# Kernel optimization log

Measured on AMD Instinct MI355X. Metric: run time of the kernel, lower is better.

Reference implementation:

```python
import jax, jax.numpy as jnp
import numpy as np

NUM_QUBITS = 10
LAYERS = 8
DIM = 2 ** NUM_QUBITS  # 1024


def _build_entangling(nq: int) -> jnp.ndarray:
    """Static chain-of-CNOTs entangling block, D x D complex64."""
    I = np.eye(2)
    cnot = np.array([[1, 0, 0, 0], [0, 1, 0, 0], [0, 0, 0, 1], [0, 0, 1, 0]], dtype=np.float64)
    M = np.eye(2 ** nq)
    layers = []
    for i in range(nq - 1):
        mats = [I] * nq
        mats[i] = cnot
        del mats[i + 1]
        out = np.eye(1)
        for m in mats:
            out = np.kron(out, m)
        layers.append(out)
    for L in reversed(layers):
        M = L @ M
    return jnp.asarray(M, dtype=jnp.complex64)


ENTANGLING = _build_entangling(NUM_QUBITS)


def _r3(angles):
    # angles: [B, 3] (omega, theta, phi) -> [B, 2, 2] complex64 R3 gate
    omega, theta, phi = angles[:, 0], angles[:, 1], angles[:, 2]
    c = jnp.cos(theta / 2).astype(jnp.complex64)
    s = jnp.sin(theta / 2).astype(jnp.complex64)
    m11 = jnp.exp(-0.5j * (phi + omega)) * c
    m12 = -jnp.exp(0.5j * (phi - omega)) * s
    m21 = jnp.exp(-0.5j * (phi - omega)) * s
    m22 = jnp.exp(0.5j * (phi + omega)) * c
    return jnp.stack([jnp.stack([m11, m12], -1), jnp.stack([m21, m22], -1)], -2)


def _batched_kron(a, b):
    # a: [B, m, n], b: [B, p, q] -> [B, m*p, n*q]
    B = a.shape[0]
    return jnp.einsum('bij,bkl->bikjl', a, b).reshape(B, a.shape[1] * b.shape[1], a.shape[2] * b.shape[2])


def _rotation_block(angles):
    # angles: [copies, num_qubits, 3] -> [copies, D, D] complex64
    out = _r3(angles[:, 0])
    for q in range(1, NUM_QUBITS):
        out = _batched_kron(out, _r3(angles[:, q]))
    return out


def setup_inputs() -> dict:
    key = jax.random.key(0)
    k1, k2 = jax.random.split(key)
    inp = jax.random.normal(k1, (128, DIM), dtype=jnp.float32)
    params = jax.random.normal(k2, (32, LAYERS, NUM_QUBITS, 3), dtype=jnp.float32)
    return {"input": inp, "params": params}


def reference(input, params):
    copies = params.shape[0]
    batch = input.shape[0] // copies
    M0 = jnp.broadcast_to(jnp.eye(DIM, dtype=jnp.complex64), (copies, DIM, DIM))
    xs = jnp.moveaxis(params, 1, 0)  # [layers, copies, nq, 3]

    def step(M, p):
        M = jnp.matmul(_rotation_block(p), M)         # rotation layer
        M = jnp.einsum('ij,bjk->bik', ENTANGLING, M)  # entangling layer
        return M, None

    M, _ = jax.lax.scan(step, M0, xs)
    M = jnp.repeat(M, batch, axis=0)                  # [copies*batch, D, D]
    x = input.astype(jnp.complex64)
    return jnp.einsum('bij,bj->bi', M, x)
```

## Files before the change

kernel.cpp:

```cpp
#include <hip/hip_runtime.h>


#define DIM 1024
#define NQ 10
#define NLAYERS 8
#define NGATES 80

__device__ __forceinline__ unsigned short f2bf(float f) {
    unsigned int u = __float_as_uint(f);
    unsigned int r = u + 0x7FFFu + ((u >> 16) & 1u);
    return (unsigned short)(r >> 16);
}

__device__ __forceinline__ float2 cmadd2(float2 c0, float2 x0, float2 c1, float2 x1) {
    float re = c0.x * x0.x - c0.y * x0.y + c1.x * x1.x - c1.y * x1.y;
    float im = c0.x * x0.y + c0.y * x0.x + c1.x * x1.y + c1.y * x1.x;
    return make_float2(re, im);
}

template <int K>
__device__ __forceinline__ void local_gate(float2 (&a)[4], float2 m11, float2 m12,
                                           float2 m21, float2 m22) {
#pragma unroll
    for (int p = 0; p < 2; ++p) {
        const int i0 = ((p >> K) << (K + 1)) | (p & ((1 << K) - 1));
        const int i1 = i0 | (1 << K);
        const float2 a0 = a[i0], a1 = a[i1];
        a[i0] = cmadd2(m11, a0, m12, a1);
        a[i1] = cmadd2(m21, a0, m22, a1);
    }
}

template <int M>
__device__ __forceinline__ void cross_gate(float2 (&a)[4], int lane, float2 m11,
                                           float2 m12, float2 m21, float2 m22) {
    const bool hi = (lane >> M) & 1;
    const float2 cs = hi ? m22 : m11;
    const float2 co = hi ? m21 : m12;
#pragma unroll
    for (int r = 0; r < 4; ++r) {
        float2 o;
        o.x = __shfl_xor(a[r].x, 1 << M, 64);
        o.y = __shfl_xor(a[r].y, 1 << M, 64);
        a[r] = cmadd2(cs, a[r], co, o);
    }
}

__global__ __launch_bounds__(256) void
UnitaryR3Ansatz_18846316495450_kernel(const float* __restrict__ inp,
                                      const float* __restrict__ params,
                                      void* __restrict__ outp,
                                      int out_size)
{
    __shared__ float4 gates[NGATES][2];
    __shared__ float4 stA[DIM / 2];
    __shared__ float4 stB[DIM / 2];

    const int b = blockIdx.x;
    const int c = b >> 2;
    const int tid = threadIdx.x;
    const int lane = tid & 63;

    if (tid < NGATES) {
        const float* p = params + c * (NGATES * 3) + tid * 3;
        const float omega = p[0], theta = p[1], phi = p[2];
        float sh, ch;  sincosf(0.5f * theta, &sh, &ch);
        float sa, ca;  sincosf(0.5f * (phi + omega), &sa, &ca);
        float sb, cb;  sincosf(0.5f * (phi - omega), &sb, &cb);
        gates[tid][0] = make_float4(ca * ch, -sa * ch, -cb * sh, -sb * sh);
        gates[tid][1] = make_float4(cb * sh, -sb * sh, ca * ch, sa * ch);
    }

    float2 a[4];
    {
        const float4 v = ((const float4*)(inp + b * DIM))[tid];
        a[0] = make_float2(v.x, 0.f);
        a[1] = make_float2(v.y, 0.f);
        a[2] = make_float2(v.z, 0.f);
        a[3] = make_float2(v.w, 0.f);
    }

    const int xb = tid << 2;
    int zb = xb;
    zb ^= zb >> 1; zb ^= zb >> 2; zb ^= zb >> 4; zb ^= zb >> 8;
    const int  zmid = zb & 0xFC;
    const bool z8 = (zb >> 8) & 1;
    const bool z9 = (zb >> 9) & 1;
    const bool s0 = zb & 1;
    const bool s1 = zb & 2;

    __syncthreads();

    float4* buf = stA;
    for (int l = 0; l < NLAYERS; ++l) {
        float2 m11, m12, m21, m22;
#define LOADG(q) { const float4 g0 = gates[l * NQ + (q)][0]; \
                   const float4 g1 = gates[l * NQ + (q)][1]; \
                   m11 = make_float2(g0.x, g0.y); m12 = make_float2(g0.z, g0.w); \
                   m21 = make_float2(g1.x, g1.y); m22 = make_float2(g1.z, g1.w); }
        LOADG(9); local_gate<0>(a, m11, m12, m21, m22);
        LOADG(8); local_gate<1>(a, m11, m12, m21, m22);
        LOADG(7); cross_gate<0>(a, lane, m11, m12, m21, m22);
        LOADG(6); cross_gate<1>(a, lane, m11, m12, m21, m22);
        LOADG(5); cross_gate<2>(a, lane, m11, m12, m21, m22);
        LOADG(4); cross_gate<3>(a, lane, m11, m12, m21, m22);
        LOADG(3); cross_gate<4>(a, lane, m11, m12, m21, m22);
        LOADG(2); cross_gate<5>(a, lane, m11, m12, m21, m22);

        buf[tid * 2]     = make_float4(a[0].x, a[0].y, a[1].x, a[1].y);
        buf[tid * 2 + 1] = make_float4(a[2].x, a[2].y, a[3].x, a[3].y);
        __syncthreads();

        LOADG(1);
        const float2 h0 = z8 ? m21 : m11;
        const float2 h1 = z8 ? m22 : m12;
        LOADG(0);
        const float2 g0r = z9 ? m21 : m11;
        const float2 g1r = z9 ? m22 : m12;
#undef LOADG

        float2 v0[4], v1[4];
        {
            const float4 p0 = buf[(zmid) >> 1],          p1 = buf[((zmid) >> 1) + 1];
            const float4 q0 = buf[(0x100 | zmid) >> 1],  q1 = buf[((0x100 | zmid) >> 1) + 1];
            v0[0] = cmadd2(h0, make_float2(p0.x, p0.y), h1, make_float2(q0.x, q0.y));
            v0[1] = cmadd2(h0, make_float2(p0.z, p0.w), h1, make_float2(q0.z, q0.w));
            v0[2] = cmadd2(h0, make_float2(p1.x, p1.y), h1, make_float2(q1.x, q1.y));
            v0[3] = cmadd2(h0, make_float2(p1.z, p1.w), h1, make_float2(q1.z, q1.w));
        }
        {
            const float4 p0 = buf[(0x200 | zmid) >> 1],  p1 = buf[((0x200 | zmid) >> 1) + 1];
            const float4 q0 = buf[(0x300 | zmid) >> 1],  q1 = buf[((0x300 | zmid) >> 1) + 1];
            v1[0] = cmadd2(h0, make_float2(p0.x, p0.y), h1, make_float2(q0.x, q0.y));
            v1[1] = cmadd2(h0, make_float2(p0.z, p0.w), h1, make_float2(q0.z, q0.w));
            v1[2] = cmadd2(h0, make_float2(p1.x, p1.y), h1, make_float2(q1.x, q1.y));
            v1[3] = cmadd2(h0, make_float2(p1.z, p1.w), h1, make_float2(q1.z, q1.w));
        }
        float2 u[4];
#pragma unroll
        for (int j = 0; j < 4; ++j) u[j] = cmadd2(g0r, v0[j], g1r, v1[j]);

        const float2 w0 = s0 ? u[1] : u[0];
        const float2 w1 = s0 ? u[0] : u[1];
        const float2 w2 = s0 ? u[3] : u[2];
        const float2 w3 = s0 ? u[2] : u[3];
        a[0] = s1 ? w2 : w0;
        a[1] = s1 ? w3 : w1;
        a[2] = s1 ? w1 : w3;
        a[3] = s1 ? w0 : w2;

        buf = (l & 1) ? stA : stB;
    }

    if (out_size >= 2 * DIM * 128) {
        ushort2* o2 = (ushort2*)outp + (size_t)b * DIM + tid * 4;
#pragma unroll
        for (int i = 0; i < 4; ++i) {
            ushort2 v; v.x = f2bf(a[i].x); v.y = f2bf(a[i].y);
            o2[i] = v;
        }
    } else {
        ((float4*)((float*)outp + (size_t)b * DIM))[tid] =
            make_float4(a[0].x, a[1].x, a[2].x, a[3].x);
    }
}

extern "C" void kernel_launch(void* const* d_in, const int* in_sizes, int n_in,
                              void* d_out, int out_size, void* d_ws, size_t ws_size,
                              hipStream_t stream) {
    const float* inp    = (const float*)d_in[0];
    const float* params = (const float*)d_in[1];
    (void)in_sizes; (void)n_in; (void)d_ws; (void)ws_size;
    UnitaryR3Ansatz_18846316495450_kernel<<<128, 256, 0, stream>>>(inp, params, d_out, out_size);
}
```

Baseline: 69.86 us.

## Use DPP/swizzle lane exchanges, halve gate storage, swizzle LDS staging

Replaces the generic shuffle-XOR lane exchanges with DPP quad/row operations and ds_swizzle for the small strides, which avoids the LDS-routed bpermute path. Stores only the first row of each R3 gate and derives the second row from the unitary's symmetry, halving shared gate loads. Applies an XOR swizzle to the staging buffer indices to reduce LDS bank conflicts on the float4 accesses. The kernel is tiny and launch-bound (128 blocks), so total gains may be small, and the DPP row_ror/swizzle encodings must match the intended xor patterns exactly.

```diff
diff --git a/kernel.cpp b/kernel.cpp
--- a/kernel.cpp
+++ b/kernel.cpp
@@ -5,6 +5,8 @@
 #define NQ 10
 #define NLAYERS 8
 #define NGATES 80
+
+#define SWZ(j) ((j) ^ (((j) >> 3) & 1))
 
 __device__ __forceinline__ unsigned short f2bf(float f) {
     unsigned int u = __float_as_uint(f);
@@ -18,9 +20,27 @@
     return make_float2(re, im);
 }
 
+template <int M>
+__device__ __forceinline__ float lxor(float v) {
+    if constexpr (M == 0)
+        return __int_as_float(__builtin_amdgcn_update_dpp(0, __float_as_int(v), 0xB1, 0xF, 0xF, true));
+    else if constexpr (M == 1)
+        return __int_as_float(__builtin_amdgcn_update_dpp(0, __float_as_int(v), 0x4E, 0xF, 0xF, true));
+    else if constexpr (M == 3)
+        return __int_as_float(__builtin_amdgcn_update_dpp(0, __float_as_int(v), 0x128, 0xF, 0xF, true));
+    else if constexpr (M == 2)
+        return __int_as_float(__builtin_amdgcn_ds_swizzle(__float_as_int(v), 0x101F));
+    else if constexpr (M == 4)
+        return __int_as_float(__builtin_amdgcn_ds_swizzle(__float_as_int(v), 0x401F));
+    else
+        return __shfl_xor(v, 32, 64);
+}
+
+
 template <int K>
-__device__ __forceinline__ void local_gate(float2 (&a)[4], float2 m11, float2 m12,
-                                           float2 m21, float2 m22) {
+__device__ __forceinline__ void local_gate(float2 (&a)[4], float2 m11, float2 m12) {
+    const float2 m21 = make_float2(-m12.x, m12.y);
+    const float2 m22 = make_float2(m11.x, -m11.y);
 #pragma unroll
     for (int p = 0; p < 2; ++p) {
         const int i0 = ((p >> K) << (K + 1)) | (p & ((1 << K) - 1));
@@ -32,16 +52,15 @@
 }
 
 template <int M>
-__device__ __forceinline__ void cross_gate(float2 (&a)[4], int lane, float2 m11,
-                                           float2 m12, float2 m21, float2 m22) {
+__device__ __forceinline__ void cross_gate(float2 (&a)[4], int lane, float2 m11, float2 m12) {
     const bool hi = (lane >> M) & 1;
-    const float2 cs = hi ? m22 : m11;
-    const float2 co = hi ? m21 : m12;
+    const float2 cs = make_float2(m11.x, hi ? -m11.y : m11.y);
+    const float2 co = make_float2(hi ? -m12.x : m12.x, m12.y);
 #pragma unroll
     for (int r = 0; r < 4; ++r) {
         float2 o;
-        o.x = __shfl_xor(a[r].x, 1 << M, 64);
-        o.y = __shfl_xor(a[r].y, 1 << M, 64);
+        o.x = lxor<M>(a[r].x);
+        o.y = lxor<M>(a[r].y);
         a[r] = cmadd2(cs, a[r], co, o);
     }
 }
@@ -52,7 +71,7 @@
                                       void* __restrict__ outp,
                                       int out_size)
 {
-    __shared__ float4 gates[NGATES][2];
+    __shared__ float4 gates[NGATES];
     __shared__ float4 stA[DIM / 2];
     __shared__ float4 stB[DIM / 2];
 
@@ -67,8 +86,7 @@
         float sh, ch;  sincosf(0.5f * theta, &sh, &ch);
         float sa, ca;  sincosf(0.5f * (phi + omega), &sa, &ca);
         float sb, cb;  sincosf(0.5f * (phi - omega), &sb, &cb);
-        gates[tid][0] = make_float4(ca * ch, -sa * ch, -cb * sh, -sb * sh);
-        gates[tid][1] = make_float4(cb * sh, -sb * sh, ca * ch, sa * ch);
+        gates[tid] = make_float4(ca * ch, -sa * ch, -cb * sh, -sb * sh);
     }
 
     float2 a[4];
@@ -84,6 +102,7 @@
     int zb = xb;
     zb ^= zb >> 1; zb ^= zb >> 2; zb ^= zb >> 4; zb ^= zb >> 8;
     const int  zmid = zb & 0xFC;
+    const int  j0 = zmid >> 1;
     const bool z8 = (zb >> 8) & 1;
     const bool z9 = (zb >> 9) & 1;
     const bool s0 = zb & 1;
@@ -93,44 +112,42 @@
 
     float4* buf = stA;
     for (int l = 0; l < NLAYERS; ++l) {
-        float2 m11, m12, m21, m22;
-#define LOADG(q) { const float4 g0 = gates[l * NQ + (q)][0]; \
-                   const float4 g1 = gates[l * NQ + (q)][1]; \
-                   m11 = make_float2(g0.x, g0.y); m12 = make_float2(g0.z, g0.w); \
-                   m21 = make_float2(g1.x, g1.y); m22 = make_float2(g1.z, g1.w); }
-        LOADG(9); local_gate<0>(a, m11, m12, m21, m22);
-        LOADG(8); local_gate<1>(a, m11, m12, m21, m22);
-        LOADG(7); cross_gate<0>(a, lane, m11, m12, m21, m22);
-        LOADG(6); cross_gate<1>(a, lane, m11, m12, m21, m22);
-        LOADG(5); cross_gate<2>(a, lane, m11, m12, m21, m22);
-        LOADG(4); cross_gate<3>(a, lane, m11, m12, m21, m22);
-        LOADG(3); cross_gate<4>(a, lane, m11, m12, m21, m22);
-        LOADG(2); cross_gate<5>(a, lane, m11, m12, m21, m22);
+        float2 m11, m12;
+#define LOADG(q) { const float4 g = gates[l * NQ + (q)]; \
+                   m11 = make_float2(g.x, g.y); m12 = make_float2(g.z, g.w); }
+        LOADG(9); local_gate<0>(a, m11, m12);
+        LOADG(8); local_gate<1>(a, m11, m12);
+        LOADG(7); cross_gate<0>(a, lane, m11, m12);
+        LOADG(6); cross_gate<1>(a, lane, m11, m12);
+        LOADG(5); cross_gate<2>(a, lane, m11, m12);
+        LOADG(4); cross_gate<3>(a, lane, m11, m12);
+        LOADG(3); cross_gate<4>(a, lane, m11, m12);
+        LOADG(2); cross_gate<5>(a, lane, m11, m12);
 
-        buf[tid * 2]     = make_float4(a[0].x, a[0].y, a[1].x, a[1].y);
-        buf[tid * 2 + 1] = make_float4(a[2].x, a[2].y, a[3].x, a[3].y);
+        buf[SWZ(tid * 2)]     = make_float4(a[0].x, a[0].y, a[1].x, a[1].y);
+        buf[SWZ(tid * 2 + 1)] = make_float4(a[2].x, a[2].y, a[3].x, a[3].y);
         __syncthreads();
 
         LOADG(1);
-        const float2 h0 = z8 ? m21 : m11;
-        const float2 h1 = z8 ? m22 : m12;
+        const float2 h0 = z8 ? make_float2(-m12.x, m12.y) : m11;
+        const float2 h1 = z8 ? make_float2(m11.x, -m11.y) : m12;
         LOADG(0);
-        const float2 g0r = z9 ? m21 : m11;
-        const float2 g1r = z9 ? m22 : m12;
+        const float2 g0r = z9 ? make_float2(-m12.x, m12.y) : m11;
+        const float2 g1r = z9 ? make_float2(m11.x, -m11.y) : m12;
 #undef LOADG
 
         float2 v0[4], v1[4];
         {
-            const float4 p0 = buf[(zmid) >> 1],          p1 = buf[((zmid) >> 1) + 1];
-            const float4 q0 = buf[(0x100 | zmid) >> 1],  q1 = buf[((0x100 | zmid) >> 1) + 1];
+            const float4 p0 = buf[SWZ(j0)],         p1 = buf[SWZ(j0 + 1)];
+            const float4 q0 = buf[SWZ(j0 + 0x80)],  q1 = buf[SWZ(j0 + 0x81)];
             v0[0] = cmadd2(h0, make_float2(p0.x, p0.y), h1, make_float2(q0.x, q0.y));
             v0[1] = cmadd2(h0, make_float2(p0.z, p0.w), h1, make_float2(q0.z, q0.w));
             v0[2] = cmadd2(h0, make_float2(p1.x, p1.y), h1, make_float2(q1.x, q1.y));
             v0[3] = cmadd2(h0, make_float2(p1.z, p1.w), h1, make_float2(q1.z, q1.w));
         }
         {
-            const float4 p0 = buf[(0x200 | zmid) >> 1],  p1 = buf[((0x200 | zmid) >> 1) + 1];
-            const float4 q0 = buf[(0x300 | zmid) >> 1],  q1 = buf[((0x300 | zmid) >> 1) + 1];
+            const float4 p0 = buf[SWZ(j0 + 0x100)], p1 = buf[SWZ(j0 + 0x101)];
+            const float4 q0 = buf[SWZ(j0 + 0x180)], q1 = buf[SWZ(j0 + 0x181)];
             v1[0] = cmadd2(h0, make_float2(p0.x, p0.y), h1, make_float2(q0.x, q0.y));
             v1[1] = cmadd2(h0, make_float2(p0.z, p0.w), h1, make_float2(q0.z, q0.w));
             v1[2] = cmadd2(h0, make_float2(p1.x, p1.y), h1, make_float2(q1.x, q1.y));
```

Result: faster. 66.88 us (-4.3%).
